# Kernel tuning notes

Hardware: AMD Instinct MI355X
Metric: run time of the kernel (lower is better)

The kernel has to match this reference:

```python
import jax, jax.numpy as jnp
import numpy as np

N = 50000          # atoms (nodes)
NEIGH = 12         # neighbors per atom
N_CRYS = 500       # crystals, 100 atoms each (contiguous)
H_E = 128          # h_fea_edge
H_A = 128          # h_fea_angle
N_CLS = 2
BOND_STEPS, BOND_MIN, BOND_MAX = 40, 0.0, 8.0
ANG_STEPS, ANG_MIN, ANG_MAX = 8, -1.0, 1.0


def _gbf(data, dmin, dmax, steps):
    # Gaussian basis expansion on the last (new) axis
    filters = jnp.linspace(dmin, dmax, steps, dtype=jnp.float32)
    gamma = (dmax - dmin) / steps
    return jnp.exp(-((data[..., None] - filters) ** 2) / (gamma ** 2))


def _sage_conv(x, src, dst, Wl, Wr, b):
    # PyG SAGEConv, mean aggregation:
    #   out_i = Wl @ mean_{(j->i) in E} x_j + b + Wr @ x_i
    n = x.shape[0]
    msg = x[src]                                             # [E, F] gather
    agg = jax.ops.segment_sum(msg, dst, num_segments=n)      # [N, F] scatter-add
    cnt = jax.ops.segment_sum(jnp.ones((src.shape[0],), x.dtype), dst, num_segments=n)
    agg = agg / jnp.maximum(cnt, 1.0)[:, None]
    return agg @ Wl.T + b + x @ Wr.T


def _segment_mean_pool(x, crys_idx):
    # crys_idx: [C, 2] contiguous [start, end) ranges covering [0, N)
    n = x.shape[0]
    starts = crys_idx[:, 0]
    seg_id = jnp.searchsorted(starts, jnp.arange(n), side='right') - 1
    counts = (crys_idx[:, 1] - crys_idx[:, 0]).astype(x.dtype)
    summed = jax.ops.segment_sum(x, seg_id, num_segments=crys_idx.shape[0])
    return summed / jnp.maximum(counts, 1.0)[:, None]


def setup_inputs() -> dict:
    key = jax.random.key(0)
    ks = jax.random.split(key, 24)
    in_b = BOND_STEPS * NEIGH            # 480
    in_a = ANG_STEPS * NEIGH * NEIGH     # 1152
    h_cat = H_E + H_A                    # 256

    def lin(k, fo, fi):
        return jax.random.normal(k, (fo, fi), jnp.float32) * (1.0 / np.sqrt(fi))

    atoms_per = N // N_CRYS
    starts = np.arange(N_CRYS, dtype=np.int32) * atoms_per
    crys_idx = jnp.asarray(np.stack([starts, starts + atoms_per], axis=1))

    return {
        'bond_fea': jax.random.uniform(ks[0], (N, NEIGH), jnp.float32) * BOND_MAX,
        'angle_fea': jax.random.uniform(ks[1], (N, NEIGH, NEIGH), jnp.float32) * 2.0 - 1.0,
        'species': jax.random.randint(ks[2], (N,), 0, 100, jnp.int32),
        'nbr_idx': jax.random.randint(ks[3], (N, NEIGH), 0, N, jnp.int32),
        'crys_idx': crys_idx,
        'Wl_b1': lin(ks[4], H_E, in_b), 'Wr_b1': lin(ks[5], H_E, in_b),
        'b_b1': jnp.zeros((H_E,), jnp.float32),
        'Wl_a1': lin(ks[6], H_A, in_a), 'Wr_a1': lin(ks[7], H_A, in_a),
        'b_a1': jnp.zeros((H_A,), jnp.float32),
        'Wl_b': jnp.stack([lin(ks[8], H_E, H_E), lin(ks[9], H_E, H_E)]),
        'Wr_b': jnp.stack([lin(ks[10], H_E, H_E), lin(ks[11], H_E, H_E)]),
        'b_b': jnp.zeros((2, H_E), jnp.float32),
        'Wl_a': jnp.stack([lin(ks[12], H_A, H_A), lin(ks[13], H_A, H_A)]),
        'Wr_a': jnp.stack([lin(ks[14], H_A, H_A), lin(ks[15], H_A, H_A)]),
        'b_a': jnp.zeros((2, H_A), jnp.float32),
        'W_mlp': jnp.stack([lin(ks[16], h_cat, h_cat), lin(ks[17], h_cat, h_cat)]),
        'b_mlp': jnp.zeros((2, h_cat), jnp.float32),
        'W_fc': lin(ks[18], N_CLS, h_cat),
        'b_fc': jnp.zeros((N_CLS,), jnp.float32),
    }


def reference(bond_fea, angle_fea, species, nbr_idx, crys_idx,
              Wl_b1, Wr_b1, b_b1, Wl_a1, Wr_a1, b_a1,
              Wl_b, Wr_b, b_b, Wl_a, Wr_a, b_a,
              W_mlp, b_mlp, W_fc, b_fc):
    n, neigh = nbr_idx.shape
    # get_edge_index: source = repeated node id, dest = neighbor id
    src = jnp.repeat(jnp.arange(n, dtype=nbr_idx.dtype), neigh)   # [N*neigh]
    dst = nbr_idx.reshape(-1)                                     # [N*neigh]

    # GBF expansions, flattened per node
    edge_fea = _gbf(bond_fea, BOND_MIN, BOND_MAX, BOND_STEPS).reshape(n, -1)    # [N, 480]
    ang_fea = _gbf(angle_fea, ANG_MIN, ANG_MAX, ANG_STEPS).reshape(n, -1)       # [N, 1152]

    # first SAGE layers (dropout_prob = 0 -> identity)
    b_out = jax.nn.relu(_sage_conv(edge_fea, src, dst, Wl_b1, Wr_b1, b_b1))
    a_out = jax.nn.relu(_sage_conv(ang_fea, src, dst, Wl_a1, Wr_a1, b_a1))

    # stacked SAGE layers (n_conv - 1 = 2 each)
    for i in range(Wl_b.shape[0]):
        b_out = jax.nn.relu(_sage_conv(b_out, src, dst, Wl_b[i], Wr_b[i], b_b[i]))
    for i in range(Wl_a.shape[0]):
        a_out = jax.nn.relu(_sage_conv(a_out, src, dst, Wl_a[i], Wr_a[i], b_a[i]))

    crys_fea = jnp.concatenate([b_out, a_out], axis=1)   # [N, 256]
    crys_fea = _segment_mean_pool(crys_fea, crys_idx)     # [C, 256]

    for i in range(W_mlp.shape[0]):
        crys_fea = crys_fea @ W_mlp[i].T + b_mlp[i]

    return crys_fea @ W_fc.T + b_fc                       # [C, n_classification]
```

## Files before the change

kernel.cpp:

```cpp
#include <hip/hip_runtime.h>

typedef _Float16 f16;
typedef _Float16 f16x8 __attribute__((ext_vector_type(8)));
typedef float f32x4 __attribute__((ext_vector_type(4)));

#define N_ATOMS 50000
#define NEIGH   12
#define NEDGE   (N_ATOMS * NEIGH)
#define NCRYS   500
#define NBLK    196

__device__ __forceinline__ void gld_lds16(const void* g, void* l) {
  __builtin_amdgcn_global_load_lds(
      (const __attribute__((address_space(1))) unsigned int*)g,
      (__attribute__((address_space(3))) unsigned int*)l, 16, 0, 0);
}

typedef f16 AsT[3][4][256][8];
typedef f16 BsT[3][4][128][8];

#define WAITVM(vm)                                                        \
  asm volatile("s_waitcnt vmcnt(" #vm ") lgkmcnt(0)" ::: "memory");       \
  __builtin_amdgcn_sched_barrier(0);                                      \
  __builtin_amdgcn_s_barrier();                                           \
  __builtin_amdgcn_sched_barrier(0)

#define ENDBAR                                                            \
  __builtin_amdgcn_sched_barrier(0);                                      \
  __builtin_amdgcn_s_barrier()

template <int MODE, int K>
__device__ __forceinline__ void gemm1_body(
    const float* __restrict__ Asrc, const f16* __restrict__ Wcat,
    f16* __restrict__ P, f16* __restrict__ Q, int n, AsT& As, BsT& Bs) {
  constexpr int CIN = (MODE == 1) ? 12 : 144;
  constexpr int NT = K / 32;
  constexpr float G2I = (MODE == 1) ? 25.0f : 16.0f;
  constexpr float DLT = (MODE == 1) ? (8.0f / 39.0f) : (2.0f / 7.0f);
  constexpr float C1 = 2.0f * G2I * DLT;
  constexpr float C2 = G2I * DLT * DLT;
  constexpr int RUN = (MODE == 1) ? 4 : 8;
  const float S = __expf(-2.0f * C2);

  const int tid = threadIdx.x;
  const int lane = tid & 63;
  const int wid = tid >> 6;
  const int wr = wid >> 1;
  const int wc = wid & 1;
  const int row0 = blockIdx.x * 256;
  const int half = blockIdx.y;
  const f16* Wh = Wcat + (size_t)half * 128 * K;
  f16* outp = half ? Q : P;

  const int bcol = tid & 127;
  const int bkb = tid >> 7;
  const int sArow = tid & 255;
  const int sAkb0 = tid >> 8;
  int arow = row0 + sArow;
  if (arow >= n) arow = n - 1;

  f32x4 acc[4][4];
#pragma unroll
  for (int m = 0; m < 4; ++m)
#pragma unroll
    for (int q = 0; q < 4; ++q) acc[m][q] = (f32x4)0.f;

  auto daddr = [&](int t, int p) -> const float* {
    int kb = sAkb0 + 2 * p;
    int kg0 = t * 32 + kb * 8;
    int jn = (MODE == 1) ? kg0 / 40 : (kg0 >> 3);
    return &Asrc[(size_t)arow * CIN + jn];
  };
  auto bload = [&](int t) {
    gld_lds16(Wh + (size_t)bcol * K + t * 32 + bkb * 8, &Bs[t % 3][bkb][bcol][0]);
  };
  auto expwrite = [&](int t, const float* d2) {
#pragma unroll
    for (int p = 0; p < 2; ++p) {
      int kb = sAkb0 + 2 * p;
      int kg0 = t * 32 + kb * 8;
      float d = d2[p];
      int kk0;
      if constexpr (MODE == 1) {
        int jn = kg0 / 40;
        kk0 = kg0 - jn * 40;
      } else {
        kk0 = 0;
      }
      f16 v[8];
#pragma unroll
      for (int h = 0; h < 8 / RUN; ++h) {
        float f0 = (float)(kk0 + h * RUN) * DLT + (MODE == 2 ? -1.0f : 0.0f);
        float u = d - f0;
        float g = __expf(-G2I * u * u);
        float ratio = __expf(C1 * u - C2);
        v[h * RUN] = (f16)g;
#pragma unroll
        for (int j = 1; j < RUN; ++j) {
          g *= ratio;
          ratio *= S;
          v[h * RUN + j] = (f16)g;
        }
      }
      *(f16x8*)&As[t % 3][kb][sArow][0] = *(const f16x8*)v;
    }
  };

  float dA[2], dB[2];
  bload(0);
  bload(1);
  dA[0] = *daddr(2, 0);
  dA[1] = *daddr(2, 1);
  {
    float d0[2] = {*daddr(0, 0), *daddr(0, 1)};
    expwrite(0, d0);
    float d1[2] = {*daddr(1, 0), *daddr(1, 1)};
    expwrite(1, d1);
  }

  for (int t = 0; t < NT; ++t) {
    if (t + 2 < NT) bload(t + 2);
    if (t + 3 < NT) {
      dB[0] = *daddr(t + 3, 0);
      dB[1] = *daddr(t + 3, 1);
    }
    if (t + 2 < NT) expwrite(t + 2, dA);
    if (t < NT - 3) {
      WAITVM(3);
    } else {
      WAITVM(0);
    }
    const int buf = t % 3;
    const int kb = lane >> 4;
    const int r16 = lane & 15;
    f16x8 a[4], b[4];
#pragma unroll
    for (int m = 0; m < 4; ++m)
      a[m] = *(const f16x8*)&As[buf][kb][wr * 64 + m * 16 + r16][0];
#pragma unroll
    for (int q = 0; q < 4; ++q)
      b[q] = *(const f16x8*)&Bs[buf][kb][wc * 64 + q * 16 + r16][0];
#pragma unroll
    for (int m = 0; m < 4; ++m)
#pragma unroll
      for (int q = 0; q < 4; ++q)
        acc[m][q] =
            __builtin_amdgcn_mfma_f32_16x16x32_f16(a[m], b[q], acc[m][q], 0, 0, 0);
    ENDBAR;
    dA[0] = dB[0];
    dA[1] = dB[1];
  }

  const int crow = (lane >> 4) * 4;
  const int ccol = lane & 15;
#pragma unroll
  for (int m = 0; m < 4; ++m) {
#pragma unroll
    for (int r = 0; r < 4; ++r) {
      int row = row0 + wr * 64 + m * 16 + crow + r;
      if (row < n) {
#pragma unroll
        for (int q = 0; q < 4; ++q)
          outp[(size_t)row * 128 + wc * 64 + q * 16 + ccol] = (f16)acc[m][q][r];
      }
    }
  }
}

__global__ __launch_bounds__(512) void gemm1all(
    const float* __restrict__ angle, const f16* __restrict__ Wa,
    f16* __restrict__ Pa, f16* __restrict__ Qa,
    const float* __restrict__ bond, const f16* __restrict__ Wb,
    f16* __restrict__ Pb, f16* __restrict__ Qb, int n) {
  __shared__ __align__(16) AsT As;
  __shared__ __align__(16) BsT Bs;
  if (blockIdx.z == 0)
    gemm1_body<2, 1152>(angle, Wa, Pa, Qa, n, As, Bs);
  else
    gemm1_body<1, 480>(bond, Wb, Pb, Qb, n, As, Bs);
}

__global__ __launch_bounds__(512) void gemmL(
    f16* __restrict__ axb, f16* __restrict__ axa, const f16* __restrict__ Wall,
    const float* __restrict__ bb, const float* __restrict__ ba, int lidx, int n) {
  __shared__ __align__(16) AsT As;
  __shared__ __align__(16) BsT Bs;
  const int path = blockIdx.y;
  f16* ax = path ? axa : axb;
  const f16* W = Wall + (size_t)(path * 2 + lidx) * 32768;
  const float* bias = (path ? ba : bb) + lidx * 128;

  const int tid = threadIdx.x;
  const int lane = tid & 63;
  const int wid = tid >> 6;
  const int wr = wid >> 1;
  const int wc = wid & 1;
  const int row0 = blockIdx.x * 256;

  const int bcol = tid & 127;
  const int bkb = tid >> 7;
  const int sArow = tid & 255;
  const int sAkb0 = tid >> 8;
  int arow = row0 + sArow;
  if (arow >= n) arow = n - 1;

  f32x4 acc[4][4];
#pragma unroll
  for (int m = 0; m < 4; ++m)
#pragma unroll
    for (int q = 0; q < 4; ++q) acc[m][q] = (f32x4)0.f;

  auto stage = [&](int buf, int t) {
    int k0 = t * 32;
    gld_lds16(W + (size_t)bcol * 256 + k0 + bkb * 8, &Bs[buf][bkb][bcol][0]);
#pragma unroll
    for (int p = 0; p < 2; ++p) {
      int kb = sAkb0 + 2 * p;
      gld_lds16(ax + (size_t)arow * 256 + k0 + kb * 8, &As[buf][kb][sArow][0]);
    }
  };

  stage(0, 0);
  stage(1, 1);
  for (int t = 0; t < 8; ++t) {
    if (t + 2 < 8) stage((t + 2) % 3, t + 2);
    if (t < 6) {
      WAITVM(6);
    } else if (t == 6) {
      WAITVM(3);
    } else {
      WAITVM(0);
    }
    const int buf = t % 3;
    const int kb = lane >> 4;
    const int r16 = lane & 15;
    f16x8 a[4], b[4];
#pragma unroll
    for (int m = 0; m < 4; ++m)
      a[m] = *(const f16x8*)&As[buf][kb][wr * 64 + m * 16 + r16][0];
#pragma unroll
    for (int q = 0; q < 4; ++q)
      b[q] = *(const f16x8*)&Bs[buf][kb][wc * 64 + q * 16 + r16][0];
#pragma unroll
    for (int m = 0; m < 4; ++m)
#pragma unroll
      for (int q = 0; q < 4; ++q)
        acc[m][q] =
            __builtin_amdgcn_mfma_f32_16x16x32_f16(a[m], b[q], acc[m][q], 0, 0, 0);
    ENDBAR;
  }

  const int crow = (lane >> 4) * 4;
  const int ccol = lane & 15;
#pragma unroll
  for (int m = 0; m < 4; ++m) {
#pragma unroll
    for (int r = 0; r < 4; ++r) {
      int row = row0 + wr * 64 + m * 16 + crow + r;
      if (row < n) {
#pragma unroll
        for (int q = 0; q < 4; ++q) {
          int col = wc * 64 + q * 16 + ccol;
          float v = acc[m][q][r] + bias[col];
          ax[(size_t)row * 256 + 128 + col] = (f16)fmaxf(v, 0.0f);
        }
      }
    }
  }
}

__global__ void cvtW(const float* __restrict__ Wl, const float* __restrict__ Wr,
                     f16* __restrict__ outp, int K) {
  int c = blockIdx.y;
  int k = blockIdx.x * 256 + threadIdx.x;
  if (k < K)
    outp[(size_t)c * K + k] =
        (f16)((c < 128) ? Wl[(size_t)c * K + k] : Wr[(size_t)(c - 128) * K + k]);
}

__global__ void cvtW_small(const float* __restrict__ Wl_b, const float* __restrict__ Wr_b,
                           const float* __restrict__ Wl_a, const float* __restrict__ Wr_a,
                           f16* __restrict__ outp) {
  int idx = blockIdx.x * 256 + threadIdx.x;
  int l = idx >> 15;
  int c = (idx >> 8) & 127;
  int k = idx & 255;
  const float* Wl = (l < 2) ? Wl_b + (size_t)l * 16384 : Wl_a + (size_t)(l - 2) * 16384;
  const float* Wr = (l < 2) ? Wr_b + (size_t)l * 16384 : Wr_a + (size_t)(l - 2) * 16384;
  float v = (k < 128) ? Wl[(size_t)c * 128 + k] : Wr[(size_t)c * 128 + (k - 128)];
  outp[idx] = (f16)v;
}

__global__ void k_count(const int* __restrict__ nbr, int* __restrict__ deg) {
  int e = blockIdx.x * 256 + threadIdx.x;
  if (e < NEDGE) atomicAdd(&deg[nbr[e]], 1);
}
__global__ void k_scan1(const int* __restrict__ deg, int* __restrict__ rowptr,
                        int* __restrict__ bsum) {
  __shared__ int s[256];
  int t = threadIdx.x, i = blockIdx.x * 256 + t;
  int v = (i < N_ATOMS) ? deg[i] : 0;
  s[t] = v;
  __syncthreads();
  for (int off = 1; off < 256; off <<= 1) {
    int x = (t >= off) ? s[t - off] : 0;
    __syncthreads();
    s[t] += x;
    __syncthreads();
  }
  if (i < N_ATOMS) rowptr[i] = s[t] - v;
  if (t == 255) bsum[blockIdx.x] = s[255];
}
__global__ void k_scan2(int* __restrict__ bsum) {
  __shared__ int s[256];
  int t = threadIdx.x;
  int v = (t < NBLK) ? bsum[t] : 0;
  s[t] = v;
  __syncthreads();
  for (int off = 1; off < 256; off <<= 1) {
    int x = (t >= off) ? s[t - off] : 0;
    __syncthreads();
    s[t] += x;
    __syncthreads();
  }
  if (t < NBLK) bsum[t] = s[t] - v;
}
__global__ void k_scan3(int* __restrict__ rowptr, const int* __restrict__ bsum) {
  int i = blockIdx.x * 256 + threadIdx.x;
  if (i < N_ATOMS) rowptr[i] += bsum[blockIdx.x];
  if (i == 0) rowptr[N_ATOMS] = NEDGE;
}
__global__ void k_fill(const int* __restrict__ nbr, const int* __restrict__ rowptr,
                       int* __restrict__ cursor, int* __restrict__ eidx) {
  int e = blockIdx.x * 256 + threadIdx.x;
  if (e < NEDGE) {
    int dst = nbr[e];
    int pos = rowptr[dst] + atomicAdd(&cursor[dst], 1);
    eidx[pos] = (e / NEIGH) << 8;
  }
}

__global__ __launch_bounds__(256) void gather_fin1(
    const f16* __restrict__ Pb, const f16* __restrict__ Qb,
    const f16* __restrict__ Pa, const f16* __restrict__ Qa,
    const int* __restrict__ rowptr, const int* __restrict__ eidx,
    const float* __restrict__ bias_b, const float* __restrict__ bias_a,
    f16* __restrict__ axb, f16* __restrict__ axa) {
  const int path = blockIdx.y;
  const char* Pc = (const char*)(path ? Pa : Pb);
  const f16* Q = path ? Qa : Qb;
  const float* bias = path ? bias_a : bias_b;
  f16* ax = path ? axa : axb;
  const int t = threadIdx.x;
  const int a = blockIdx.x * 16 + (t >> 4);
  const int g = (t & 15) * 8;
  const unsigned gb = (unsigned)(t & 15) * 16;
  const int s0 = rowptr[a], s1 = rowptr[a + 1];
  float acc[8];
#pragma unroll
  for (int u = 0; u < 8; ++u) acc[u] = 0.f;
  int j = s0;
  for (; j + 8 <= s1; j += 8) {
    f16x8 v[8];
#pragma unroll
    for (int u = 0; u < 8; ++u)
      v[u] = *(const f16x8*)(Pc + (size_t)((unsigned)eidx[j + u] + gb));
    f16x8 s = ((v[0] + v[1]) + (v[2] + v[3])) + ((v[4] + v[5]) + (v[6] + v[7]));
#pragma unroll
    for (int c = 0; c < 8; ++c) acc[c] += (float)s[c];
  }
  for (; j + 4 <= s1; j += 4) {
    f16x8 v0 = *(const f16x8*)(Pc + (size_t)((unsigned)eidx[j] + gb));
    f16x8 v1 = *(const f16x8*)(Pc + (size_t)((unsigned)eidx[j + 1] + gb));
    f16x8 v2 = *(const f16x8*)(Pc + (size_t)((unsigned)eidx[j + 2] + gb));
    f16x8 v3 = *(const f16x8*)(Pc + (size_t)((unsigned)eidx[j + 3] + gb));
    f16x8 s = (v0 + v1) + (v2 + v3);
#pragma unroll
    for (int c = 0; c < 8; ++c) acc[c] += (float)s[c];
  }
  for (; j < s1; ++j) {
    f16x8 v = *(const f16x8*)(Pc + (size_t)((unsigned)eidx[j] + gb));
#pragma unroll
    for (int c = 0; c < 8; ++c) acc[c] += (float)v[c];
  }
  f16x8 q = *(const f16x8*)&Q[(size_t)a * 128 + g];
  float inv = 1.0f / fmaxf((float)(s1 - s0), 1.0f);
  f16 outv[8];
#pragma unroll
  for (int u = 0; u < 8; ++u) {
    float v = acc[u] * inv + bias[g + u] + (float)q[u];
    outv[u] = (f16)fmaxf(v, 0.0f);
  }
  *(f16x8*)&ax[(size_t)a * 256 + 128 + g] = *(const f16x8*)outv;
}

__global__ __launch_bounds__(256) void gather_mean(
    f16* __restrict__ axb, f16* __restrict__ axa,
    const int* __restrict__ rowptr, const int* __restrict__ eidx) {
  f16* ax = blockIdx.y ? axa : axb;
  const char* axc = (const char*)ax;
  const int t = threadIdx.x;
  const int a = blockIdx.x * 16 + (t >> 4);
  const int g = (t & 15) * 8;
  const unsigned gb = 256u + (unsigned)(t & 15) * 16;
  const int s0 = rowptr[a], s1 = rowptr[a + 1];
  float acc[8];
#pragma unroll
  for (int u = 0; u < 8; ++u) acc[u] = 0.f;
  int j = s0;
  for (; j + 8 <= s1; j += 8) {
    f16x8 v[8];
#pragma unroll
    for (int u = 0; u < 8; ++u)
      v[u] = *(const f16x8*)(axc + (size_t)(((unsigned)eidx[j + u] << 1) + gb));
    f16x8 s = ((v[0] + v[1]) + (v[2] + v[3])) + ((v[4] + v[5]) + (v[6] + v[7]));
#pragma unroll
    for (int c = 0; c < 8; ++c) acc[c] += (float)s[c];
  }
  for (; j + 4 <= s1; j += 4) {
    f16x8 v0 = *(const f16x8*)(axc + (size_t)(((unsigned)eidx[j] << 1) + gb));
    f16x8 v1 = *(const f16x8*)(axc + (size_t)(((unsigned)eidx[j + 1] << 1) + gb));
    f16x8 v2 = *(const f16x8*)(axc + (size_t)(((unsigned)eidx[j + 2] << 1) + gb));
    f16x8 v3 = *(const f16x8*)(axc + (size_t)(((unsigned)eidx[j + 3] << 1) + gb));
    f16x8 s = (v0 + v1) + (v2 + v3);
#pragma unroll
    for (int c = 0; c < 8; ++c) acc[c] += (float)s[c];
  }
  for (; j < s1; ++j) {
    f16x8 v = *(const f16x8*)(axc + (size_t)(((unsigned)eidx[j] << 1) + gb));
#pragma unroll
    for (int c = 0; c < 8; ++c) acc[c] += (float)v[c];
  }
  float inv = 1.0f / fmaxf((float)(s1 - s0), 1.0f);
  f16 outv[8];
#pragma unroll
  for (int u = 0; u < 8; ++u) outv[u] = (f16)(acc[u] * inv);
  *(f16x8*)&ax[(size_t)a * 256 + g] = *(const f16x8*)outv;
}

__global__ __launch_bounds__(256) void head_kernel(
    const f16* __restrict__ axb, const f16* __restrict__ axa,
    const int* __restrict__ crys, const float* __restrict__ W_mlp,
    const float* __restrict__ b_mlp, const float* __restrict__ W_fc,
    const float* __restrict__ b_fc, float* __restrict__ outp) {
  __shared__ float sh0[256], sh1[256];
  const int cry = blockIdx.x, c = threadIdx.x;
  const int s = crys[2 * cry], e = crys[2 * cry + 1];
  const f16* src = (c < 128) ? axb : axa;
  const int ch = c & 127;
  float sum = 0.f;
  for (int r = s; r < e; ++r) sum += (float)src[(size_t)r * 256 + 128 + ch];
  sh0[c] = sum / fmaxf((float)(e - s), 1.0f);
  __syncthreads();
  {
    const float* wrow = W_mlp + (size_t)c * 256;
    float s2 = b_mlp[c];
#pragma unroll 8
    for (int k = 0; k < 256; k += 4) {
      float4 w = *(const float4*)&wrow[k];
      s2 += sh0[k] * w.x + sh0[k + 1] * w.y + sh0[k + 2] * w.z + sh0[k + 3] * w.w;
    }
    sh1[c] = s2;
  }
  __syncthreads();
  {
    const float* wrow = W_mlp + 65536 + (size_t)c * 256;
    float s2 = b_mlp[256 + c];
#pragma unroll 8
    for (int k = 0; k < 256; k += 4) {
      float4 w = *(const float4*)&wrow[k];
      s2 += sh1[k] * w.x + sh1[k + 1] * w.y + sh1[k + 2] * w.z + sh1[k + 3] * w.w;
    }
    sh0[c] = s2;
  }
  __syncthreads();
  if (c < 2) {
    const float* wrow = W_fc + c * 256;
    float s2 = b_fc[c];
    for (int k = 0; k < 256; ++k) s2 += sh0[k] * wrow[k];
    outp[cry * 2 + c] = s2;
  }
}

extern "C" void kernel_launch(void* const* d_in, const int* in_sizes, int n_in,
                              void* d_out, int out_size, void* d_ws, size_t ws_size,
                              hipStream_t stream) {
  const float* bond  = (const float*)d_in[0];
  const float* angle = (const float*)d_in[1];
  const int*   nbr   = (const int*)d_in[3];
  const int*   crys  = (const int*)d_in[4];
  const float* Wl_b1 = (const float*)d_in[5];
  const float* Wr_b1 = (const float*)d_in[6];
  const float* b_b1  = (const float*)d_in[7];
  const float* Wl_a1 = (const float*)d_in[8];
  const float* Wr_a1 = (const float*)d_in[9];
  const float* b_a1  = (const float*)d_in[10];
  const float* Wl_b  = (const float*)d_in[11];
  const float* Wr_b  = (const float*)d_in[12];
  const float* b_b   = (const float*)d_in[13];
  const float* Wl_a  = (const float*)d_in[14];
  const float* Wr_a  = (const float*)d_in[15];
  const float* b_a   = (const float*)d_in[16];
  const float* W_mlp = (const float*)d_in[17];
  const float* b_mlp = (const float*)d_in[18];
  const float* W_fc  = (const float*)d_in[19];
  const float* b_fc  = (const float*)d_in[20];

  char* w = (char*)d_ws;
  auto alloc = [&](size_t bytes) {
    void* p = (void*)w;
    w += (bytes + 255) & ~(size_t)255;
    return p;
  };
  f16* axb = (f16*)alloc((size_t)N_ATOMS * 256 * 2);
  f16* axa = (f16*)alloc((size_t)N_ATOMS * 256 * 2);
  f16* Pb  = (f16*)alloc((size_t)N_ATOMS * 128 * 2);
  f16* Qb  = (f16*)alloc((size_t)N_ATOMS * 128 * 2);
  f16* Pa  = (f16*)alloc((size_t)N_ATOMS * 128 * 2);
  f16* Qa  = (f16*)alloc((size_t)N_ATOMS * 128 * 2);
  f16* Wb1c = (f16*)alloc((size_t)256 * 480 * 2);
  f16* Wa1c = (f16*)alloc((size_t)256 * 1152 * 2);
  f16* Wsm  = (f16*)alloc((size_t)4 * 128 * 256 * 2);
  int* deg    = (int*)alloc((size_t)2 * N_ATOMS * 4);
  int* cursor = deg + N_ATOMS;
  int* rowptr = (int*)alloc((size_t)(N_ATOMS + 1) * 4);
  int* eidx   = (int*)alloc((size_t)NEDGE * 4);
  int* bsum   = (int*)alloc(256 * 4);

  cvtW<<<dim3(2, 256), 256, 0, stream>>>(Wl_b1, Wr_b1, Wb1c, 480);
  cvtW<<<dim3(5, 256), 256, 0, stream>>>(Wl_a1, Wr_a1, Wa1c, 1152);
  cvtW_small<<<512, 256, 0, stream>>>(Wl_b, Wr_b, Wl_a, Wr_a, Wsm);

  hipMemsetAsync(deg, 0, (size_t)2 * N_ATOMS * 4, stream);
  k_count<<<(NEDGE + 255) / 256, 256, 0, stream>>>(nbr, deg);
  k_scan1<<<NBLK, 256, 0, stream>>>(deg, rowptr, bsum);
  k_scan2<<<1, 256, 0, stream>>>(bsum);
  k_scan3<<<NBLK, 256, 0, stream>>>(rowptr, bsum);
  k_fill<<<(NEDGE + 255) / 256, 256, 0, stream>>>(nbr, rowptr, cursor, eidx);

  const int GT = (N_ATOMS + 255) / 256;
  const int AG = N_ATOMS / 16;

  gemm1all<<<dim3(GT, 2, 2), 512, 0, stream>>>(angle, Wa1c, Pa, Qa,
                                               bond, Wb1c, Pb, Qb, N_ATOMS);
  gather_fin1<<<dim3(AG, 2), 256, 0, stream>>>(Pb, Qb, Pa, Qa, rowptr, eidx,
                                               b_b1, b_a1, axb, axa);

  for (int l = 0; l < 2; ++l) {
    gather_mean<<<dim3(AG, 2), 256, 0, stream>>>(axb, axa, rowptr, eidx);
    gemmL<<<dim3(GT, 2), 512, 0, stream>>>(axb, axa, Wsm, b_b, b_a, l, N_ATOMS);
  }

  head_kernel<<<NCRYS, 256, 0, stream>>>(axb, axa, crys, W_mlp, b_mlp, W_fc, b_fc,
                                         (float*)d_out);
}
```

Measured before the change: 392.8 us.

## Retile first-layer GEMM to 128 rows by 256 columns to avoid duplicate GBF expansion

The first SAGE GEMM tile changes from 256 rows × 128 output columns (with a grid dimension splitting the Wl/Wr halves) to 128 rows × all 256 columns. Each block now computes both P and Q for its rows, so the Gaussian basis expansion of the A operand runs once per row instead of once per half. This removes the duplicated exp work and the duplicated reads of the raw features. In exchange, each thread issues two B loads per k-step instead of one, the vmcnt wait counts are adjusted to match, and the block count becomes about 391 per path with half the per-block row count.

```diff
diff --git a/kernel.cpp b/kernel.cpp
--- a/kernel.cpp
+++ b/kernel.cpp
@@ -16,8 +16,10 @@
       (__attribute__((address_space(3))) unsigned int*)l, 16, 0, 0);
 }
 
-typedef f16 AsT[3][4][256][8];
-typedef f16 BsT[3][4][128][8];
+typedef f16 As1T[3][4][128][8];
+typedef f16 Bs1T[3][4][256][8];
+typedef f16 AsLT[3][4][256][8];
+typedef f16 BsLT[3][4][128][8];
 
 #define WAITVM(vm)                                                        \
   asm volatile("s_waitcnt vmcnt(" #vm ") lgkmcnt(0)" ::: "memory");       \
@@ -32,7 +34,7 @@
 template <int MODE, int K>
 __device__ __forceinline__ void gemm1_body(
     const float* __restrict__ Asrc, const f16* __restrict__ Wcat,
-    f16* __restrict__ P, f16* __restrict__ Q, int n, AsT& As, BsT& Bs) {
+    f16* __restrict__ P, f16* __restrict__ Q, int n, As1T& As, Bs1T& Bs) {
   constexpr int CIN = (MODE == 1) ? 12 : 144;
   constexpr int NT = K / 32;
   constexpr float G2I = (MODE == 1) ? 25.0f : 16.0f;
@@ -45,17 +47,14 @@
   const int tid = threadIdx.x;
   const int lane = tid & 63;
   const int wid = tid >> 6;
-  const int wr = wid >> 1;
-  const int wc = wid & 1;
-  const int row0 = blockIdx.x * 256;
-  const int half = blockIdx.y;
-  const f16* Wh = Wcat + (size_t)half * 128 * K;
-  f16* outp = half ? Q : P;
-
-  const int bcol = tid & 127;
-  const int bkb = tid >> 7;
-  const int sArow = tid & 255;
-  const int sAkb0 = tid >> 8;
+  const int wr = wid >> 2;
+  const int wc = wid & 3;
+  const int row0 = blockIdx.x * 128;
+
+  const int bcol = tid & 255;
+  const int bkb0 = tid >> 8;
+  const int sArow = tid & 127;
+  const int sAkb = (tid >> 7) & 3;
   int arow = row0 + sArow;
   if (arow >= n) arow = n - 1;
 
@@ -65,68 +64,64 @@
 #pragma unroll
     for (int q = 0; q < 4; ++q) acc[m][q] = (f32x4)0.f;
 
-  auto daddr = [&](int t, int p) -> const float* {
-    int kb = sAkb0 + 2 * p;
-    int kg0 = t * 32 + kb * 8;
+  auto daddr = [&](int t) -> const float* {
+    int kg0 = t * 32 + sAkb * 8;
     int jn = (MODE == 1) ? kg0 / 40 : (kg0 >> 3);
     return &Asrc[(size_t)arow * CIN + jn];
   };
   auto bload = [&](int t) {
-    gld_lds16(Wh + (size_t)bcol * K + t * 32 + bkb * 8, &Bs[t % 3][bkb][bcol][0]);
+#pragma unroll
+    for (int p = 0; p < 2; ++p) {
+      int kb = bkb0 + 2 * p;
+      gld_lds16(Wcat + (size_t)bcol * K + t * 32 + kb * 8, &Bs[t % 3][kb][bcol][0]);
+    }
   };
-  auto expwrite = [&](int t, const float* d2) {
-#pragma unroll
-    for (int p = 0; p < 2; ++p) {
-      int kb = sAkb0 + 2 * p;
-      int kg0 = t * 32 + kb * 8;
-      float d = d2[p];
-      int kk0;
-      if constexpr (MODE == 1) {
-        int jn = kg0 / 40;
-        kk0 = kg0 - jn * 40;
-      } else {
-        kk0 = 0;
+  auto expwrite = [&](int t, float d) {
+    int kg0 = t * 32 + sAkb * 8;
+    int kk0;
+    if constexpr (MODE == 1) {
+      int jn = kg0 / 40;
+      kk0 = kg0 - jn * 40;
+    } else {
+      kk0 = 0;
+    }
+    f16 v[8];
+#pragma unroll
+    for (int h = 0; h < 8 / RUN; ++h) {
+      float f0 = (float)(kk0 + h * RUN) * DLT + (MODE == 2 ? -1.0f : 0.0f);
+      float u = d - f0;
+      float g = __expf(-G2I * u * u);
+      float ratio = __expf(C1 * u - C2);
+      v[h * RUN] = (f16)g;
+#pragma unroll
+      for (int j = 1; j < RUN; ++j) {
+        g *= ratio;
+        ratio *= S;
+        v[h * RUN + j] = (f16)g;
       }
-      f16 v[8];
-#pragma unroll
-      for (int h = 0; h < 8 / RUN; ++h) {
-        float f0 = (float)(kk0 + h * RUN) * DLT + (MODE == 2 ? -1.0f : 0.0f);
-        float u = d - f0;
-        float g = __expf(-G2I * u * u);
-        float ratio = __expf(C1 * u - C2);
-        v[h * RUN] = (f16)g;
-#pragma unroll
-        for (int j = 1; j < RUN; ++j) {
-          g *= ratio;
-          ratio *= S;
-          v[h * RUN + j] = (f16)g;
-        }
-      }
-      *(f16x8*)&As[t % 3][kb][sArow][0] = *(const f16x8*)v;
-    }
+    }
+    *(f16x8*)&As[t % 3][sAkb][sArow][0] = *(const f16x8*)v;
   };
 
-  float dA[2], dB[2];
+  float dA, dB;
   bload(0);
   bload(1);
-  dA[0] = *daddr(2, 0);
-  dA[1] = *daddr(2, 1);
+  dA = *daddr(2);
   {
-    float d0[2] = {*daddr(0, 0), *daddr(0, 1)};
+    float d0 = *daddr(0);
     expwrite(0, d0);
-    float d1[2] = {*daddr(1, 0), *daddr(1, 1)};
+    float d1 = *daddr(1);
     expwrite(1, d1);
   }
 
   for (int t = 0; t < NT; ++t) {
     if (t + 2 < NT) bload(t + 2);
-    if (t + 3 < NT) {
-      dB[0] = *daddr(t + 3, 0);
-      dB[1] = *daddr(t + 3, 1);
-    }
+    if (t + 3 < NT) dB = *daddr(t + 3);
     if (t + 2 < NT) expwrite(t + 2, dA);
-    if (t < NT - 3) {
+    if (t < NT - 2) {
       WAITVM(3);
+    } else if (t == NT - 2) {
+      WAITVM(2);
     } else {
       WAITVM(0);
     }
@@ -147,12 +142,13 @@
         acc[m][q] =
             __builtin_amdgcn_mfma_f32_16x16x32_f16(a[m], b[q], acc[m][q], 0, 0, 0);
     ENDBAR;
-    dA[0] = dB[0];
-    dA[1] = dB[1];
+    dA = dB;
   }
 
   const int crow = (lane >> 4) * 4;
   const int ccol = lane & 15;
+  f16* outp = (wc < 2) ? P : Q;
+  const int cbase = (wc & 1) * 64;
 #pragma unroll
   for (int m = 0; m < 4; ++m) {
 #pragma unroll
@@ -161,7 +157,7 @@
       if (row < n) {
 #pragma unroll
         for (int q = 0; q < 4; ++q)
-          outp[(size_t)row * 128 + wc * 64 + q * 16 + ccol] = (f16)acc[m][q][r];
+          outp[(size_t)row * 128 + cbase + q * 16 + ccol] = (f16)acc[m][q][r];
       }
     }
   }
@@ -172,9 +168,9 @@
     f16* __restrict__ Pa, f16* __restrict__ Qa,
     const float* __restrict__ bond, const f16* __restrict__ Wb,
     f16* __restrict__ Pb, f16* __restrict__ Qb, int n) {
-  __shared__ __align__(16) AsT As;
-  __shared__ __align__(16) BsT Bs;
-  if (blockIdx.z == 0)
+  __shared__ __align__(16) As1T As;
+  __shared__ __align__(16) Bs1T Bs;
+  if (blockIdx.y == 0)
     gemm1_body<2, 1152>(angle, Wa, Pa, Qa, n, As, Bs);
   else
     gemm1_body<1, 480>(bond, Wb, Pb, Qb, n, As, Bs);
@@ -183,8 +179,8 @@
 __global__ __launch_bounds__(512) void gemmL(
     f16* __restrict__ axb, f16* __restrict__ axa, const f16* __restrict__ Wall,
     const float* __restrict__ bb, const float* __restrict__ ba, int lidx, int n) {
-  __shared__ __align__(16) AsT As;
-  __shared__ __align__(16) BsT Bs;
+  __shared__ __align__(16) AsLT As;
+  __shared__ __align__(16) BsLT Bs;
   const int path = blockIdx.y;
   f16* ax = path ? axa : axb;
   const f16* W = Wall + (size_t)(path * 2 + lidx) * 32768;
@@ -538,11 +534,12 @@
   k_scan3<<<NBLK, 256, 0, stream>>>(rowptr, bsum);
   k_fill<<<(NEDGE + 255) / 256, 256, 0, stream>>>(nbr, rowptr, cursor, eidx);
 
+  const int GG = (N_ATOMS + 127) / 128;
   const int GT = (N_ATOMS + 255) / 256;
   const int AG = N_ATOMS / 16;
 
-  gemm1all<<<dim3(GT, 2, 2), 512, 0, stream>>>(angle, Wa1c, Pa, Qa,
-                                               bond, Wb1c, Pb, Qb, N_ATOMS);
+  gemm1all<<<dim3(GG, 2), 512, 0, stream>>>(angle, Wa1c, Pa, Qa,
+                                            bond, Wb1c, Pb, Qb, N_ATOMS);
   gather_fin1<<<dim3(AG, 2), 256, 0, stream>>>(Pb, Qb, Pa, Qa, rowptr, eidx,
                                                b_b1, b_a1, axb, axa);
 
```

Result: slower. 411.2 us (+4.7%).
